# Kernel optimization log

Hardware: AMD Instinct MI355X
Metric: run time of the kernel (lower is better)

The kernel has to match this reference:

```python
import jax, jax.numpy as jnp
import numpy as np

B, S, H = 16, 8192, 512

def setup_inputs() -> dict:
    key = jax.random.key(0)
    k1, k2, k3, k4, k5 = jax.random.split(key, 5)
    scale = 1.0 / np.sqrt(H)
    return {
        "encoder_outputs": jax.random.normal(k1, (B, S, H), dtype=jnp.float32),
        "query": jax.random.normal(k2, (B, H), dtype=jnp.float32),
        "W_h": jax.random.normal(k3, (H, H), dtype=jnp.float32) * scale,
        "W_q": jax.random.normal(k4, (H, H), dtype=jnp.float32) * scale,
        "v": jax.random.normal(k5, (H,), dtype=jnp.float32) * scale,
    }

def reference(encoder_outputs, query, W_h, W_q, v):
    # h_proj: (B,S,H) = enc @ W_h^T (torch Linear convention)
    h_proj = jnp.einsum('bsh,oh->bso', encoder_outputs, W_h)
    # q_proj: (B,1,H)
    q_proj = jnp.einsum('bh,oh->bo', query, W_q)[:, None, :]
    # scores: (B,S) = tanh(h_proj + q_proj) @ v
    scores = jnp.einsum('bso,o->bs', jnp.tanh(h_proj + q_proj), v)
    alpha = jax.nn.softmax(scores, axis=1)          # (B,S)
    context = jnp.einsum('bs,bsh->bh', alpha, encoder_outputs)  # (B,H)
    return (context, alpha)
```

## Files before the change

kernel.cpp:

```cpp
#include <hip/hip_runtime.h>

typedef float  f32x4  __attribute__((ext_vector_type(4)));
typedef __bf16 bf16x8 __attribute__((ext_vector_type(8)));

#define LOG2E      1.4426950408889634f
#define TWO_LOG2E  2.8853900817779268f

__device__ __forceinline__ float fast_tanh(float x) {
    float e = __builtin_amdgcn_exp2f(x * TWO_LOG2E);
    return 1.0f - 2.0f * __builtin_amdgcn_rcpf(e + 1.0f);
}

__global__ void wh_swizzle_kernel(const float* __restrict__ Wh,
                                  __bf16* __restrict__ Wswz) {
    int gid = blockIdx.x * 256 + threadIdx.x;
    int n   = gid >> 6;
    int k8  = gid & 63;
    const float* g = Wh + ((long)n << 9) + (k8 << 3);
    f32x4 f0 = *(const f32x4*)g;
    f32x4 f1 = *(const f32x4*)(g + 4);
    bf16x8 val;
    val[0] = (__bf16)f0[0]; val[1] = (__bf16)f0[1];
    val[2] = (__bf16)f0[2]; val[3] = (__bf16)f0[3];
    val[4] = (__bf16)f1[0]; val[5] = (__bf16)f1[1];
    val[6] = (__bf16)f1[2]; val[7] = (__bf16)f1[3];
    int nc = n >> 8, w = (n >> 6) & 3, nt = (n >> 4) & 3, lm = n & 15;
    int s  = k8 >> 2, q = k8 & 3;
    long chunk = (long)(((nc * 16 + s) * 16 + w * 4 + nt) * 64 + (q * 16 + lm));
    *(bf16x8*)(Wswz + (chunk << 3)) = val;
}

__global__ void qproj_kernel(const float* __restrict__ query,
                             const float* __restrict__ Wq,
                             float* __restrict__ qp) {
    int b = blockIdx.x >> 1;
    int o = ((blockIdx.x & 1) << 8) + threadIdx.x;
    const f32x4* qrow = (const f32x4*)(query + (b << 9));
    const f32x4* wrow = (const f32x4*)(Wq + ((long)o << 9));
    float acc = 0.f;
    #pragma unroll 4
    for (int i = 0; i < 128; ++i) {
        f32x4 a = qrow[i], w = wrow[i];
        acc += a[0]*w[0] + a[1]*w[1] + a[2]*w[2] + a[3]*w[3];
    }
    qp[(b << 9) + o] = acc;
}

__global__ __launch_bounds__(256, 2) void score_ctx_kernel(
    const float*  __restrict__ enc,
    const __bf16* __restrict__ Wswz,
    const float*  __restrict__ qp,
    const float*  __restrict__ v,
    float* __restrict__ alpha_out,
    float* __restrict__ ctx_acc,
    float* __restrict__ denom)
{
    __shared__ __align__(16) unsigned char ldsA[65536];
    __shared__ float score_lds[256];
    __shared__ float escore[64];

    const int  t    = threadIdx.x;
    const int  w    = t >> 6;
    const int  l    = t & 63;
    const long row0 = (long)blockIdx.x << 6;
    const int  b    = (int)(row0 >> 13);

    #pragma unroll
    for (int i = 0; i < 16; ++i) {
        int cflat = t + (i << 8);
        int m = cflat >> 6, k8 = cflat & 63;
        const float* g = enc + ((row0 + m) << 9) + (k8 << 3);
        f32x4 f0 = *(const f32x4*)g;
        f32x4 f1 = *(const f32x4*)(g + 4);
        bf16x8 val;
        val[0] = (__bf16)f0[0]; val[1] = (__bf16)f0[1];
        val[2] = (__bf16)f0[2]; val[3] = (__bf16)f0[3];
        val[4] = (__bf16)f1[0]; val[5] = (__bf16)f1[1];
        val[6] = (__bf16)f1[2]; val[7] = (__bf16)f1[3];
        int chunk = ((m >> 4) * 16 + (k8 >> 2)) * 64 +
                    ((((k8 & 3) << 4) | (m & 15)) ^ ((k8 >> 2) & 7));
        *(bf16x8*)(ldsA + (chunk << 4)) = val;
    }

    f32x4 acc[2][4][4];
    float vv[2][4];
    #pragma unroll
    for (int nc = 0; nc < 2; ++nc)
        #pragma unroll
        for (int nt = 0; nt < 4; ++nt) {
            int n = (nc << 8) + (w << 6) + (nt << 4) + (l & 15);
            float q = qp[(b << 9) + n];
            vv[nc][nt] = v[n];
            f32x4 qv = {q, q, q, q};
            #pragma unroll
            for (int mt = 0; mt < 4; ++mt) acc[nc][nt][mt] = qv;
        }

    __syncthreads();

    const bf16x8* Bg = (const bf16x8*)Wswz;
    #pragma unroll 2
    for (int s = 0; s < 16; ++s) {
        bf16x8 af[4];
        #pragma unroll
        for (int mt = 0; mt < 4; ++mt)
            af[mt] = *(const bf16x8*)(ldsA + (((((mt << 4) + s) << 6) + (l ^ (s & 7))) << 4));
        #pragma unroll
        for (int nc = 0; nc < 2; ++nc)
            #pragma unroll
            for (int nt = 0; nt < 4; ++nt) {
                bf16x8 bf = Bg[(long)((((nc << 4) + s) << 4) + (w << 2) + nt) * 64 + l];
                #pragma unroll
                for (int mt = 0; mt < 4; ++mt)
                    acc[nc][nt][mt] = __builtin_amdgcn_mfma_f32_16x16x32_bf16(
                        af[mt], bf, acc[nc][nt][mt], 0, 0, 0);
            }
    }

    float srow[16];
    #pragma unroll
    for (int i = 0; i < 16; ++i) srow[i] = 0.f;
    #pragma unroll
    for (int nc = 0; nc < 2; ++nc)
        #pragma unroll
        for (int nt = 0; nt < 4; ++nt) {
            float vn = vv[nc][nt];
            #pragma unroll
            for (int mt = 0; mt < 4; ++mt)
                #pragma unroll
                for (int r = 0; r < 4; ++r)
                    srow[mt * 4 + r] += vn * fast_tanh(acc[nc][nt][mt][r]);
        }
    #pragma unroll
    for (int i = 0; i < 16; ++i) {
        #pragma unroll
        for (int off = 1; off < 16; off <<= 1)
            srow[i] += __shfl_xor(srow[i], off, 64);
    }
    __syncthreads();
    if ((l & 15) == 0) {
        int qd = l >> 4;
        #pragma unroll
        for (int mt = 0; mt < 4; ++mt)
            #pragma unroll
            for (int r = 0; r < 4; ++r)
                score_lds[(w << 6) + (mt << 4) + (qd << 2) + r] = srow[mt * 4 + r];
    }
    __syncthreads();

    if (t < 64) {
        float sc = score_lds[t] + score_lds[64 + t] + score_lds[128 + t] + score_lds[192 + t];
        float e  = __builtin_amdgcn_exp2f(sc * LOG2E);
        alpha_out[row0 + t] = e;
        escore[t] = e;
        float ssum = e;
        #pragma unroll
        for (int off = 1; off < 64; off <<= 1) ssum += __shfl_xor(ssum, off, 64);
        if (t == 0) atomicAdd(denom + b, ssum);
    }
    __syncthreads();

    int rg = t >> 6, k8 = t & 63;
    float ca[8];
    #pragma unroll
    for (int j = 0; j < 8; ++j) ca[j] = 0.f;
    #pragma unroll
    for (int ii = 0; ii < 16; ++ii) {
        int m = (rg << 4) + ii;
        float em = escore[m];
        int chunk = ((m >> 4) * 16 + (k8 >> 2)) * 64 +
                    ((((k8 & 3) << 4) | (m & 15)) ^ ((k8 >> 2) & 7));
        bf16x8 av = *(const bf16x8*)(ldsA + (chunk << 4));
        #pragma unroll
        for (int j = 0; j < 8; ++j) ca[j] += em * (float)av[j];
    }
    __syncthreads();
    float* part = (float*)ldsA;
    #pragma unroll
    for (int j = 0; j < 8; ++j) part[t * 9 + j] = ca[j];
    __syncthreads();
    for (int h = t; h < 512; h += 256) {
        int k8h = h >> 3, j = h & 7;
        float sum = 0.f;
        #pragma unroll
        for (int r2 = 0; r2 < 4; ++r2) sum += part[((r2 << 6) | k8h) * 9 + j];
        atomicAdd(ctx_acc + ((long)b << 9) + h, sum);
    }
}

__global__ void normalize_kernel(const float* __restrict__ ctx_acc,
                                 const float* __restrict__ denom,
                                 float* __restrict__ out) {
    int i = blockIdx.x * 256 + threadIdx.x;
    if (i < 8192) {
        int b = i >> 9;
        out[i] = ctx_acc[i] / denom[b];
    } else if (i < 8192 + 131072) {
        int b = (i - 8192) >> 13;
        out[i] = out[i] / denom[b];
    }
}

extern "C" void kernel_launch(void* const* d_in, const int* in_sizes, int n_in,
                              void* d_out, int out_size, void* d_ws, size_t ws_size,
                              hipStream_t stream) {
    const float* enc   = (const float*)d_in[0];
    const float* query = (const float*)d_in[1];
    const float* Wh    = (const float*)d_in[2];
    const float* Wq    = (const float*)d_in[3];
    const float* v     = (const float*)d_in[4];
    float* out = (float*)d_out;

    char* ws = (char*)d_ws;
    float*  ctx_acc = (float*)ws;
    float*  denom   = (float*)(ws + 32768);
    float*  qp      = (float*)(ws + 32832);
    __bf16* Wswz    = (__bf16*)(ws + 65600);

    hipMemsetAsync(ws, 0, 32832, stream);
    wh_swizzle_kernel<<<128, 256, 0, stream>>>(Wh, Wswz);
    qproj_kernel<<<32, 256, 0, stream>>>(query, Wq, qp);
    score_ctx_kernel<<<2048, 256, 0, stream>>>(enc, Wswz, qp, v,
                                               out + 8192, ctx_acc, denom);
    normalize_kernel<<<544, 256, 0, stream>>>(ctx_acc, denom, out);
}
```

Measured before the change: 472.4 us.

## Use 512-thread blocks with 8 waves splitting N, new LDS swizzle, parallel qproj

```diff
diff --git a/kernel.cpp b/kernel.cpp
--- a/kernel.cpp
+++ b/kernel.cpp
@@ -9,6 +9,11 @@
 __device__ __forceinline__ float fast_tanh(float x) {
     float e = __builtin_amdgcn_exp2f(x * TWO_LOG2E);
     return 1.0f - 2.0f * __builtin_amdgcn_rcpf(e + 1.0f);
+}
+
+__device__ __forceinline__ int a_chunk(int m, int k8) {
+    return (((m >> 4) * 16 + (k8 >> 2)) << 6) +
+           ((((k8 & 3) << 4) | (m & 15)) ^ ((k8 >> 2) & 7) ^ (((k8 & 3) << 1) & 7));
 }
 
 __global__ void wh_swizzle_kernel(const float* __restrict__ Wh,
@@ -24,29 +29,28 @@
     val[2] = (__bf16)f0[2]; val[3] = (__bf16)f0[3];
     val[4] = (__bf16)f1[0]; val[5] = (__bf16)f1[1];
     val[6] = (__bf16)f1[2]; val[7] = (__bf16)f1[3];
-    int nc = n >> 8, w = (n >> 6) & 3, nt = (n >> 4) & 3, lm = n & 15;
-    int s  = k8 >> 2, q = k8 & 3;
-    long chunk = (long)(((nc * 16 + s) * 16 + w * 4 + nt) * 64 + (q * 16 + lm));
-    *(bf16x8*)(Wswz + (chunk << 3)) = val;
+    int chunk = (((n >> 4) * 16 + (k8 >> 2)) << 6) + (((k8 & 3) << 4) | (n & 15));
+    *(bf16x8*)(Wswz + ((long)chunk << 3)) = val;
 }
 
 __global__ void qproj_kernel(const float* __restrict__ query,
                              const float* __restrict__ Wq,
                              float* __restrict__ qp) {
-    int b = blockIdx.x >> 1;
-    int o = ((blockIdx.x & 1) << 8) + threadIdx.x;
-    const f32x4* qrow = (const f32x4*)(query + (b << 9));
-    const f32x4* wrow = (const f32x4*)(Wq + ((long)o << 9));
-    float acc = 0.f;
-    #pragma unroll 4
-    for (int i = 0; i < 128; ++i) {
-        f32x4 a = qrow[i], w = wrow[i];
-        acc += a[0]*w[0] + a[1]*w[1] + a[2]*w[2] + a[3]*w[3];
-    }
-    qp[(b << 9) + o] = acc;
-}
-
-__global__ __launch_bounds__(256, 2) void score_ctx_kernel(
+    int pair = (blockIdx.x << 2) + (threadIdx.x >> 6);
+    int l    = threadIdx.x & 63;
+    int b    = pair >> 9;
+    long o   = pair & 511;
+    const f32x4* q  = (const f32x4*)(query + (b << 9) + (l << 3));
+    const f32x4* wr = (const f32x4*)(Wq + (o << 9) + (l << 3));
+    f32x4 a0 = q[0], a1 = q[1], w0 = wr[0], w1 = wr[1];
+    float acc = a0[0]*w0[0] + a0[1]*w0[1] + a0[2]*w0[2] + a0[3]*w0[3]
+              + a1[0]*w1[0] + a1[1]*w1[1] + a1[2]*w1[2] + a1[3]*w1[3];
+    #pragma unroll
+    for (int off = 1; off < 64; off <<= 1) acc += __shfl_xor(acc, off, 64);
+    if (l == 0) qp[pair] = acc;
+}
+
+__global__ __launch_bounds__(512, 4) void score_ctx_kernel(
     const float*  __restrict__ enc,
     const __bf16* __restrict__ Wswz,
     const float*  __restrict__ qp,
@@ -56,7 +60,7 @@
     float* __restrict__ denom)
 {
     __shared__ __align__(16) unsigned char ldsA[65536];
-    __shared__ float score_lds[256];
+    __shared__ float score_lds[512];
     __shared__ float escore[64];
 
     const int  t    = threadIdx.x;
@@ -65,9 +69,21 @@
     const long row0 = (long)blockIdx.x << 6;
     const int  b    = (int)(row0 >> 13);
 
-    #pragma unroll
-    for (int i = 0; i < 16; ++i) {
-        int cflat = t + (i << 8);
+    f32x4 acc[4][4];
+    float vv[4];
+    #pragma unroll
+    for (int nt = 0; nt < 4; ++nt) {
+        int n = (w << 6) + (nt << 4) + (l & 15);
+        float q = qp[(b << 9) + n];
+        vv[nt] = v[n];
+        f32x4 qv = {q, q, q, q};
+        #pragma unroll
+        for (int mt = 0; mt < 4; ++mt) acc[nt][mt] = qv;
+    }
+
+    #pragma unroll
+    for (int i = 0; i < 8; ++i) {
+        int cflat = t + (i << 9);
         int m = cflat >> 6, k8 = cflat & 63;
         const float* g = enc + ((row0 + m) << 9) + (k8 << 3);
         f32x4 f0 = *(const f32x4*)g;
@@ -77,24 +93,8 @@
         val[2] = (__bf16)f0[2]; val[3] = (__bf16)f0[3];
         val[4] = (__bf16)f1[0]; val[5] = (__bf16)f1[1];
         val[6] = (__bf16)f1[2]; val[7] = (__bf16)f1[3];
-        int chunk = ((m >> 4) * 16 + (k8 >> 2)) * 64 +
-                    ((((k8 & 3) << 4) | (m & 15)) ^ ((k8 >> 2) & 7));
-        *(bf16x8*)(ldsA + (chunk << 4)) = val;
-    }
-
-    f32x4 acc[2][4][4];
-    float vv[2][4];
-    #pragma unroll
-    for (int nc = 0; nc < 2; ++nc)
-        #pragma unroll
-        for (int nt = 0; nt < 4; ++nt) {
-            int n = (nc << 8) + (w << 6) + (nt << 4) + (l & 15);
-            float q = qp[(b << 9) + n];
-            vv[nc][nt] = v[n];
-            f32x4 qv = {q, q, q, q};
-            #pragma unroll
-            for (int mt = 0; mt < 4; ++mt) acc[nc][nt][mt] = qv;
-        }
+        *(bf16x8*)(ldsA + (a_chunk(m, k8) << 4)) = val;
+    }
 
     __syncthreads();
 
@@ -102,42 +102,38 @@
     #pragma unroll 2
     for (int s = 0; s < 16; ++s) {
         bf16x8 af[4];
+        int lowr = l ^ (s & 7) ^ (((l >> 4) << 1) & 7);
         #pragma unroll
         for (int mt = 0; mt < 4; ++mt)
-            af[mt] = *(const bf16x8*)(ldsA + (((((mt << 4) + s) << 6) + (l ^ (s & 7))) << 4));
-        #pragma unroll
-        for (int nc = 0; nc < 2; ++nc)
-            #pragma unroll
-            for (int nt = 0; nt < 4; ++nt) {
-                bf16x8 bf = Bg[(long)((((nc << 4) + s) << 4) + (w << 2) + nt) * 64 + l];
-                #pragma unroll
-                for (int mt = 0; mt < 4; ++mt)
-                    acc[nc][nt][mt] = __builtin_amdgcn_mfma_f32_16x16x32_bf16(
-                        af[mt], bf, acc[nc][nt][mt], 0, 0, 0);
-            }
-    }
-
-    float srow[16];
-    #pragma unroll
-    for (int i = 0; i < 16; ++i) srow[i] = 0.f;
-    #pragma unroll
-    for (int nc = 0; nc < 2; ++nc)
+            af[mt] = *(const bf16x8*)(ldsA + (((((mt << 4) + s) << 6) + lowr) << 4));
         #pragma unroll
         for (int nt = 0; nt < 4; ++nt) {
-            float vn = vv[nc][nt];
+            bf16x8 bf = Bg[((((w << 2) + nt) * 16 + s) << 6) + l];
             #pragma unroll
             for (int mt = 0; mt < 4; ++mt)
-                #pragma unroll
-                for (int r = 0; r < 4; ++r)
-                    srow[mt * 4 + r] += vn * fast_tanh(acc[nc][nt][mt][r]);
+                acc[nt][mt] = __builtin_amdgcn_mfma_f32_16x16x32_bf16(
+                    af[mt], bf, acc[nt][mt], 0, 0, 0);
         }
+    }
+
+    float srow[16];
+    #pragma unroll
+    for (int i = 0; i < 16; ++i) srow[i] = 0.f;
+    #pragma unroll
+    for (int nt = 0; nt < 4; ++nt) {
+        float vn = vv[nt];
+        #pragma unroll
+        for (int mt = 0; mt < 4; ++mt)
+            #pragma unroll
+            for (int r = 0; r < 4; ++r)
+                srow[mt * 4 + r] += vn * fast_tanh(acc[nt][mt][r]);
+    }
     #pragma unroll
     for (int i = 0; i < 16; ++i) {
         #pragma unroll
         for (int off = 1; off < 16; off <<= 1)
             srow[i] += __shfl_xor(srow[i], off, 64);
     }
-    __syncthreads();
     if ((l & 15) == 0) {
         int qd = l >> 4;
         #pragma unroll
@@ -149,8 +145,10 @@
     __syncthreads();
 
     if (t < 64) {
-        float sc = score_lds[t] + score_lds[64 + t] + score_lds[128 + t] + score_lds[192 + t];
-        float e  = __builtin_amdgcn_exp2f(sc * LOG2E);
+        float sc = 0.f;
+        #pragma unroll
+        for (int ww = 0; ww < 8; ++ww) sc += score_lds[(ww << 6) + t];
+        float e = __builtin_amdgcn_exp2f(sc * LOG2E);
         alpha_out[row0 + t] = e;
         escore[t] = e;
         float ssum = e;
@@ -160,17 +158,14 @@
     }
     __syncthreads();
 
-    int rg = t >> 6, k8 = t & 63;
     float ca[8];
     #pragma unroll
     for (int j = 0; j < 8; ++j) ca[j] = 0.f;
     #pragma unroll
-    for (int ii = 0; ii < 16; ++ii) {
-        int m = (rg << 4) + ii;
+    for (int ii = 0; ii < 8; ++ii) {
+        int m = (w << 3) + ii;
         float em = escore[m];
-        int chunk = ((m >> 4) * 16 + (k8 >> 2)) * 64 +
-                    ((((k8 & 3) << 4) | (m & 15)) ^ ((k8 >> 2) & 7));
-        bf16x8 av = *(const bf16x8*)(ldsA + (chunk << 4));
+        bf16x8 av = *(const bf16x8*)(ldsA + (a_chunk(m, l) << 4));
         #pragma unroll
         for (int j = 0; j < 8; ++j) ca[j] += em * (float)av[j];
     }
@@ -179,11 +174,12 @@
     #pragma unroll
     for (int j = 0; j < 8; ++j) part[t * 9 + j] = ca[j];
     __syncthreads();
-    for (int h = t; h < 512; h += 256) {
+    {
+        int h = t;
         int k8h = h >> 3, j = h & 7;
         float sum = 0.f;
         #pragma unroll
-        for (int r2 = 0; r2 < 4; ++r2) sum += part[((r2 << 6) | k8h) * 9 + j];
+        for (int rg = 0; rg < 8; ++rg) sum += part[((rg << 6) | k8h) * 9 + j];
         atomicAdd(ctx_acc + ((long)b << 9) + h, sum);
     }
 }
@@ -219,8 +215,8 @@
 
     hipMemsetAsync(ws, 0, 32832, stream);
     wh_swizzle_kernel<<<128, 256, 0, stream>>>(Wh, Wswz);
-    qproj_kernel<<<32, 256, 0, stream>>>(query, Wq, qp);
-    score_ctx_kernel<<<2048, 256, 0, stream>>>(enc, Wswz, qp, v,
+    qproj_kernel<<<2048, 256, 0, stream>>>(query, Wq, qp);
+    score_ctx_kernel<<<2048, 512, 0, stream>>>(enc, Wswz, qp, v,
                                                out + 8192, ctx_acc, denom);
     normalize_kernel<<<544, 256, 0, stream>>>(ctx_acc, denom, out);
 }
```

Measured after the change: 424.5 us. -10.1%, faster.
